# Kernel optimization log

Measured on AMD Instinct MI355X. Metric: run time of the kernel, lower is better.

The kernel has to match this reference:

```python
import jax, jax.numpy as jnp
import numpy as np

N = 8192
IN_F = 512
OUT_F = 128
ALPHA = 0.2  # leaky relu negative slope
NEG_BIG = -1e10
RND_SCALE = 1e5


def setup_inputs() -> dict:
    key = jax.random.key(0)
    k1, k2, k3, k4, k5 = jax.random.split(key, 5)
    h = jax.random.normal(k1, (N, IN_F), dtype=jnp.float32)
    adj = jax.random.randint(k2, (N, N), 0, 2, dtype=jnp.int32)
    W = jax.random.normal(k3, (IN_F, OUT_F), dtype=jnp.float32) * 0.05
    a = jax.random.normal(k4, (2 * OUT_F, 1), dtype=jnp.float32) * 0.1
    # rnd in original is 1e5*(rand-0.5); same distribution here
    rnd = RND_SCALE * (jax.random.uniform(k5, (N, OUT_F), dtype=jnp.float32) - 0.5)
    return {"h": h, "adj": adj, "W": W, "a": a, "rnd": rnd}


def reference(h, adj, W, a, rnd):
    Wh = h @ W                              # [N, OUT_F]
    Wh1 = Wh @ a[:OUT_F, :]                 # [N, 1]
    Wh2 = Wh @ a[OUT_F:, :]                 # [N, 1]
    e = jax.nn.leaky_relu(Wh1 + Wh2.T, negative_slope=ALPHA)  # [N, N]
    attention = jnp.where(adj > 0, e, NEG_BIG)
    attention = jax.nn.softmax(attention, axis=1)
    h_prime = attention @ Wh                # [N, OUT_F]
    h_prime = (h_prime + rnd) / RND_SCALE
    return jax.nn.elu(h_prime)
```

## Files before the change

### kernel.cpp

```cpp
#include <hip/hip_runtime.h>

#define N 8192
#define IN_F 512
#define OUT_F 128
#define NW (N / 8)
#define SPLITK 8
#define KC 1024
#define LOG2E 1.4426950408889634f
#define LN2 0.6931471805599453f

typedef __attribute__((ext_vector_type(4))) float f32x4;
typedef __attribute__((ext_vector_type(8))) short bf16x8;
typedef __attribute__((ext_vector_type(8))) unsigned short u16x8;
typedef __attribute__((ext_vector_type(4))) int i32x4;

__device__ __forceinline__ short f2bf(float f) {
    union { float f; unsigned u; } c; c.f = f;
    unsigned r = c.u + 0x7FFFu + ((c.u >> 16) & 1u);
    return (short)(r >> 16);
}

__device__ __forceinline__ float exp2fast(float x) {
#if __has_builtin(__builtin_amdgcn_exp2f)
    return __builtin_amdgcn_exp2f(x);
#else
    return __expf(x * LN2);
#endif
}

__device__ __forceinline__ void load_lds16(const void* g, void* l) {
    __builtin_amdgcn_global_load_lds((const __attribute__((address_space(1))) unsigned*)g,
                                     (__attribute__((address_space(3))) unsigned*)l,
                                     16, 0, 0);
}

__global__ __launch_bounds__(256) void prep(const int* __restrict__ adj,
                                            unsigned char* __restrict__ maskR,
                                            const float* __restrict__ W,
                                            short* __restrict__ WT) {
    if (blockIdx.x >= 2048) {
        int idx = (blockIdx.x - 2048) * 256 + threadIdx.x;
        int n = idx & (OUT_F - 1);
        int k = idx >> 7;
        WT[(size_t)n * IN_F + k] = f2bf(W[idx]);
        return;
    }
    const int wave = threadIdx.x >> 6, lane = threadIdx.x & 63;
    const size_t m = (size_t)blockIdx.x * 4 + wave;
    const i32x4* ap = (const i32x4*)(adj + m * N);
    unsigned char* mp = maskR + m * NW;
#pragma unroll 4
    for (int it = 0; it < 16; it++) {
        int b4 = it * 128 + lane * 2;
        i32x4 a0 = __builtin_nontemporal_load(ap + b4);
        i32x4 a1 = __builtin_nontemporal_load(ap + b4 + 1);
        unsigned b = (unsigned)(a0.x > 0) | ((unsigned)(a0.y > 0) << 1) |
                     ((unsigned)(a0.z > 0) << 2) | ((unsigned)(a0.w > 0) << 3) |
                     ((unsigned)(a1.x > 0) << 4) | ((unsigned)(a1.y > 0) << 5) |
                     ((unsigned)(a1.z > 0) << 6) | ((unsigned)(a1.w > 0) << 7);
        mp[it * 64 + lane] = (unsigned char)b;
    }
}

__global__ __launch_bounds__(256) void gemm_hW(const float* __restrict__ h,
                                               const short* __restrict__ WT,
                                               const float* __restrict__ a,
                                               short* __restrict__ WhT,
                                               float* __restrict__ sOut,
                                               float* __restrict__ tOut) {
    const int tid = threadIdx.x;
    const int wave = tid >> 6, lane = tid & 63;
    const int row16 = lane & 15, kgrp = lane >> 4;
    const int m0 = blockIdx.x * 16;
    const int kbase = wave * 128;

    f32x4 acc[8] = {};
    const float4* hp = (const float4*)(h + (size_t)(m0 + row16) * IN_F + kbase);

#pragma unroll
    for (int kk = 0; kk < 128; kk += 32) {
        float4 u0 = hp[kk / 4 + kgrp * 2];
        float4 u1 = hp[kk / 4 + kgrp * 2 + 1];
        bf16x8 af;
        af[0] = f2bf(u0.x); af[1] = f2bf(u0.y); af[2] = f2bf(u0.z); af[3] = f2bf(u0.w);
        af[4] = f2bf(u1.x); af[5] = f2bf(u1.y); af[6] = f2bf(u1.z); af[7] = f2bf(u1.w);
#pragma unroll
        for (int nt = 0; nt < 8; nt++) {
            bf16x8 bf_ = *(const bf16x8*)(WT + (size_t)(nt * 16 + row16) * IN_F + kbase + kk + kgrp * 8);
            acc[nt] = __builtin_amdgcn_mfma_f32_16x16x32_bf16(af, bf_, acc[nt], 0, 0, 0);
        }
    }

    __shared__ float red[4][16][132];
#pragma unroll
    for (int nt = 0; nt < 8; nt++)
#pragma unroll
        for (int r = 0; r < 4; r++)
            red[wave][kgrp * 4 + r][nt * 16 + row16] = acc[nt][r];
    __syncthreads();

    const int row = tid >> 4, seg = tid & 15;
    float v[8];
#pragma unroll
    for (int e = 0; e < 8; e++) {
        int c = seg * 8 + e;
        v[e] = red[0][row][c] + red[1][row][c] + red[2][row][c] + red[3][row][c];
    }
    float sp = 0.f, tp = 0.f;
#pragma unroll
    for (int e = 0; e < 8; e++) {
        sp += v[e] * a[seg * 8 + e];
        tp += v[e] * a[OUT_F + seg * 8 + e];
    }
    sp += __shfl_xor(sp, 1); tp += __shfl_xor(tp, 1);
    sp += __shfl_xor(sp, 2); tp += __shfl_xor(tp, 2);
    sp += __shfl_xor(sp, 4); tp += __shfl_xor(tp, 4);
    sp += __shfl_xor(sp, 8); tp += __shfl_xor(tp, 8);
    if (seg == 0) {
        sOut[m0 + row] = sp * LOG2E;
        tOut[m0 + row] = tp * LOG2E;
    }
#pragma unroll
    for (int e = 0; e < 8; e++)
        WhT[(size_t)(seg * 8 + e) * N + m0 + row] = f2bf(v[e]);
}

__global__ __launch_bounds__(256, 4) void attn(const unsigned char* __restrict__ maskR,
                                               const short* __restrict__ WhT,
                                               const float* __restrict__ s,
                                               const float* __restrict__ t,
                                               unsigned short* __restrict__ num,
                                               float* __restrict__ lpart) {
    const int tid = threadIdx.x;
    const int wave = tid >> 6, lane = tid & 63;
    const int row16 = lane & 15, kgrp = lane >> 4;
    const int kb = blockIdx.x & 7;
    const int mb = blockIdx.x >> 3;
    const int m0 = mb * 64 + wave * 16;
    const int m  = m0 + row16;
    const int ks = kb * KC;

    __shared__ short Bs[2][2][128 * 32];
    __shared__ float tl[KC];

    for (int i = tid; i < KC; i += 256) tl[i] = t[ks + i];

    const float s_m = s[m];
    const int4* mp = (const int4*)(maskR + (size_t)m * NW + (ks >> 3));
    int4 mcur = mp[0], mnxt = mp[1];

    auto stageB = [&](int sup, int par) {
        const int k0 = ks + sup * 64;
#pragma unroll
        for (int d = 0; d < 2; d++)
#pragma unroll
            for (int q = 0; q < 2; q++) {
                int nrow = wave * 32 + q * 16 + (lane >> 2);
                const short* g = WhT + (size_t)nrow * N + k0 + d * 32 + (lane & 3) * 8;
                load_lds16(g, &Bs[par][d][(wave * 32 + q * 16) * 32]);
            }
    };

    f32x4 acc[8] = {};
    float lsum = 0.f;

    stageB(0, 0);
    __syncthreads();

    for (int sp2 = 0; sp2 < 8; sp2++) {
#pragma unroll
        for (int ss = 0; ss < 2; ss++) {
            const int sp = sp2 * 2 + ss;
            const int par = sp & 1;
            if (sp + 1 < 16) stageB(sp + 1, par ^ 1);
#pragma unroll
            for (int d = 0; d < 2; d++) {
                const int g = sp * 2 + d;
                const unsigned dw = (unsigned)((const int*)&mcur)[ss * 2 + d];
                const unsigned mbyte = (dw >> (kgrp * 8)) & 0xFFu;

                const float* tp = tl + g * 32 + kgrp * 8;
                float4 tA = *(const float4*)tp;
                float4 tB = *(const float4*)(tp + 4);
                float tv[8] = { tA.x, tA.y, tA.z, tA.w, tB.x, tB.y, tB.z, tB.w };

                bf16x8 bfr[8];
                const short* base = &Bs[par][d][0];
#pragma unroll
                for (int ni = 0; ni < 8; ni++)
                    bfr[ni] = *(const bf16x8*)(base + (ni * 16 + row16) * 32 + kgrp * 8);

                unsigned pu[8];
#pragma unroll
                for (int e = 0; e < 8; e++) {
                    float x = s_m + tv[e];
                    x = fmaxf(x, 0.2f * x);
                    float p = exp2fast(x);
                    unsigned u = __float_as_uint(p) & 0xFFFF0000u;
                    u = ((mbyte >> e) & 1u) ? u : 0u;
                    lsum += __uint_as_float(u);
                    pu[e] = u;
                }
                bf16x8 af;
                unsigned* au = (unsigned*)&af;
#pragma unroll
                for (int q = 0; q < 4; q++) au[q] = (pu[2 * q] >> 16) | pu[2 * q + 1];
#pragma unroll
                for (int ni = 0; ni < 8; ni++)
                    acc[ni] = __builtin_amdgcn_mfma_f32_16x16x32_bf16(af, bfr[ni], acc[ni], 0, 0, 0);
            }
            __syncthreads();
        }
        mcur = mnxt;
        if (sp2 + 2 < 8) mnxt = mp[sp2 + 2];
    }

    {
        float v = lsum;
        v += __shfl_xor(v, 16);
        v += __shfl_xor(v, 32);
        if (kgrp == 0) lpart[(size_t)kb * N + m] = v;
    }

    unsigned short* np_ = num + ((size_t)kb * N + m0) * OUT_F;
#pragma unroll
    for (int ni = 0; ni < 8; ni++) {
        int n = ni * 16 + row16;
#pragma unroll
        for (int r = 0; r < 4; r++)
            np_[(size_t)(kgrp * 4 + r) * OUT_F + n] = (unsigned short)f2bf(acc[ni][r]);
    }
}

__global__ __launch_bounds__(256) void finalize(const unsigned short* __restrict__ num,
                                                const float* __restrict__ lpart,
                                                const float* __restrict__ rnd,
                                                float* __restrict__ out) {
    int idx = blockIdx.x * 256 + threadIdx.x;
    int m = idx >> 4;
    int c = (idx & 15) * 8;
    size_t g = (size_t)m * OUT_F + c;

    float nm[8] = {};
#pragma unroll
    for (int bk = 0; bk < SPLITK; bk++) {
        u16x8 v = *(const u16x8*)(num + (size_t)bk * N * OUT_F + g);
#pragma unroll
        for (int e = 0; e < 8; e++) nm[e] += __uint_as_float((unsigned)v[e] << 16);
    }
    float l = 0.f;
#pragma unroll
    for (int bk = 0; bk < SPLITK; bk++) l += lpart[(size_t)bk * N + m];
    float inv = 1.f / fmaxf(l, 1e-30f);

    float4 r0 = *(const float4*)(rnd + g);
    float4 r1 = *(const float4*)(rnd + g + 4);
    float rv[8] = { r0.x, r0.y, r0.z, r0.w, r1.x, r1.y, r1.z, r1.w };
    float ov[8];
#pragma unroll
    for (int e = 0; e < 8; e++) {
        float x = (nm[e] * inv + rv[e]) * 1e-5f;
        ov[e] = x > 0.f ? x : __expf(x) - 1.f;
    }
    *(float4*)(out + g)     = make_float4(ov[0], ov[1], ov[2], ov[3]);
    *(float4*)(out + g + 4) = make_float4(ov[4], ov[5], ov[6], ov[7]);
}

extern "C" void kernel_launch(void* const* d_in, const int* in_sizes, int n_in,
                              void* d_out, int out_size, void* d_ws, size_t ws_size,
                              hipStream_t stream) {
    const float* h   = (const float*)d_in[0];
    const int*   adj = (const int*)d_in[1];
    const float* W   = (const float*)d_in[2];
    const float* a   = (const float*)d_in[3];
    const float* rnd = (const float*)d_in[4];
    float* out = (float*)d_out;

    char* w = (char*)d_ws;
    short* WT    = (short*)(w);
    short* WhT   = (short*)(w + 131072);
    float* sv    = (float*)(w + 2228224);
    float* tv    = (float*)(w + 2260992);
    float* lpart = (float*)(w + 2293760);
    unsigned char* maskR = (unsigned char*)(w + 2555904);
    unsigned short* num  = (unsigned short*)(w + 10944512);

    prep    <<<2304, 256, 0, stream>>>(adj, maskR, W, WT);
    gemm_hW <<<512, 256, 0, stream>>>(h, WT, a, WhT, sv, tv);
    attn    <<<1024, 256, 0, stream>>>(maskR, WhT, sv, tv, num, lpart);
    finalize<<<(N * OUT_F / 8) / 256, 256, 0, stream>>>(num, lpart, rnd, out);
}
```

Before: 410.0 us.

## Fuse adjacency mask reading into attention kernel, drop bitmask prep pass

Removes the separate pass that packs the int32 adjacency matrix into a bitmask and instead has the attention kernel read the raw adj values directly, prefetched one stage ahead with nontemporal loads. This cuts the extra write and read of the packed mask and one kernel's worth of work, so the 256 MB adjacency is streamed once. The catch is that the attention kernel now pulls 32x more mask bytes per element and carries more live registers for the prefetch buffers, which may hurt occupancy or stall the MFMA loop.

```diff
diff --git a/kernel.cpp b/kernel.cpp
--- a/kernel.cpp
+++ b/kernel.cpp
@@ -3,7 +3,6 @@
 #define N 8192
 #define IN_F 512
 #define OUT_F 128
-#define NW (N / 8)
 #define SPLITK 8
 #define KC 1024
 #define LOG2E 1.4426950408889634f
@@ -34,32 +33,12 @@
                                      16, 0, 0);
 }
 
-__global__ __launch_bounds__(256) void prep(const int* __restrict__ adj,
-                                            unsigned char* __restrict__ maskR,
-                                            const float* __restrict__ W,
+__global__ __launch_bounds__(256) void prep(const float* __restrict__ W,
                                             short* __restrict__ WT) {
-    if (blockIdx.x >= 2048) {
-        int idx = (blockIdx.x - 2048) * 256 + threadIdx.x;
-        int n = idx & (OUT_F - 1);
-        int k = idx >> 7;
-        WT[(size_t)n * IN_F + k] = f2bf(W[idx]);
-        return;
-    }
-    const int wave = threadIdx.x >> 6, lane = threadIdx.x & 63;
-    const size_t m = (size_t)blockIdx.x * 4 + wave;
-    const i32x4* ap = (const i32x4*)(adj + m * N);
-    unsigned char* mp = maskR + m * NW;
-#pragma unroll 4
-    for (int it = 0; it < 16; it++) {
-        int b4 = it * 128 + lane * 2;
-        i32x4 a0 = __builtin_nontemporal_load(ap + b4);
-        i32x4 a1 = __builtin_nontemporal_load(ap + b4 + 1);
-        unsigned b = (unsigned)(a0.x > 0) | ((unsigned)(a0.y > 0) << 1) |
-                     ((unsigned)(a0.z > 0) << 2) | ((unsigned)(a0.w > 0) << 3) |
-                     ((unsigned)(a1.x > 0) << 4) | ((unsigned)(a1.y > 0) << 5) |
-                     ((unsigned)(a1.z > 0) << 6) | ((unsigned)(a1.w > 0) << 7);
-        mp[it * 64 + lane] = (unsigned char)b;
-    }
+    int idx = blockIdx.x * 256 + threadIdx.x;
+    int n = idx & (OUT_F - 1);
+    int k = idx >> 7;
+    WT[(size_t)n * IN_F + k] = f2bf(W[idx]);
 }
 
 __global__ __launch_bounds__(256) void gemm_hW(const float* __restrict__ h,
@@ -125,7 +104,7 @@
         WhT[(size_t)(seg * 8 + e) * N + m0 + row] = f2bf(v[e]);
 }
 
-__global__ __launch_bounds__(256, 4) void attn(const unsigned char* __restrict__ maskR,
+__global__ __launch_bounds__(256, 4) void attn(const int* __restrict__ adj,
                                                const short* __restrict__ WhT,
                                                const float* __restrict__ s,
                                                const float* __restrict__ t,
@@ -143,11 +122,18 @@
     __shared__ short Bs[2][2][128 * 32];
     __shared__ float tl[KC];
 
+    const i32x4* ap = (const i32x4*)(adj + (size_t)m * N + ks);
+    const int abase = kgrp * 2;
+
+    i32x4 ab[2][4];
+#pragma unroll
+    for (int d = 0; d < 2; d++)
+#pragma unroll
+        for (int hh = 0; hh < 2; hh++)
+            ab[0][d * 2 + hh] = __builtin_nontemporal_load(ap + d * 8 + abase + hh);
+
     for (int i = tid; i < KC; i += 256) tl[i] = t[ks + i];
-
     const float s_m = s[m];
-    const int4* mp = (const int4*)(maskR + (size_t)m * NW + (ks >> 3));
-    int4 mcur = mp[0], mnxt = mp[1];
 
     auto stageB = [&](int sup, int par) {
         const int k0 = ks + sup * 64;
@@ -167,17 +153,25 @@
     stageB(0, 0);
     __syncthreads();
 
-    for (int sp2 = 0; sp2 < 8; sp2++) {
+    for (int spo = 0; spo < 8; spo++) {
 #pragma unroll
         for (int ss = 0; ss < 2; ss++) {
-            const int sp = sp2 * 2 + ss;
-            const int par = sp & 1;
-            if (sp + 1 < 16) stageB(sp + 1, par ^ 1);
+            const int sp = spo * 2 + ss;
+            const int par = ss;
+            if (sp + 1 < 16) {
+#pragma unroll
+                for (int d = 0; d < 2; d++)
+#pragma unroll
+                    for (int hh = 0; hh < 2; hh++)
+                        ab[ss ^ 1][d * 2 + hh] =
+                            __builtin_nontemporal_load(ap + (sp + 1) * 16 + d * 8 + abase + hh);
+                stageB(sp + 1, par ^ 1);
+            }
 #pragma unroll
             for (int d = 0; d < 2; d++) {
                 const int g = sp * 2 + d;
-                const unsigned dw = (unsigned)((const int*)&mcur)[ss * 2 + d];
-                const unsigned mbyte = (dw >> (kgrp * 8)) & 0xFFu;
+                const i32x4 a0 = ab[ss][d * 2 + 0];
+                const i32x4 a1 = ab[ss][d * 2 + 1];
 
                 const float* tp = tl + g * 32 + kgrp * 8;
                 float4 tA = *(const float4*)tp;
@@ -190,29 +184,31 @@
                 for (int ni = 0; ni < 8; ni++)
                     bfr[ni] = *(const bf16x8*)(base + (ni * 16 + row16) * 32 + kgrp * 8);
 
-                unsigned pu[8];
-#pragma unroll
-                for (int e = 0; e < 8; e++) {
-                    float x = s_m + tv[e];
-                    x = fmaxf(x, 0.2f * x);
-                    float p = exp2fast(x);
-                    unsigned u = __float_as_uint(p) & 0xFFFF0000u;
-                    u = ((mbyte >> e) & 1u) ? u : 0u;
-                    lsum += __uint_as_float(u);
-                    pu[e] = u;
-                }
                 bf16x8 af;
                 unsigned* au = (unsigned*)&af;
 #pragma unroll
-                for (int q = 0; q < 4; q++) au[q] = (pu[2 * q] >> 16) | pu[2 * q + 1];
+                for (int q = 0; q < 4; q++) {
+                    const int e0 = 2 * q, e1 = 2 * q + 1;
+                    float x0 = s_m + tv[e0];
+                    float x1 = s_m + tv[e1];
+                    x0 = fmaxf(x0, 0.2f * x0);
+                    x1 = fmaxf(x1, 0.2f * x1);
+                    unsigned u0 = __float_as_uint(exp2fast(x0)) & 0xFFFF0000u;
+                    unsigned u1 = __float_as_uint(exp2fast(x1)) & 0xFFFF0000u;
+                    const int av0 = (e0 < 4) ? a0[e0] : a1[e0 - 4];
+                    const int av1 = (e1 < 4) ? a0[e1] : a1[e1 - 4];
+                    u0 = av0 > 0 ? u0 : 0u;
+                    u1 = av1 > 0 ? u1 : 0u;
+                    lsum += __uint_as_float(u0);
+                    lsum += __uint_as_float(u1);
+                    au[q] = (u0 >> 16) | u1;
+                }
 #pragma unroll
                 for (int ni = 0; ni < 8; ni++)
                     acc[ni] = __builtin_amdgcn_mfma_f32_16x16x32_bf16(af, bfr[ni], acc[ni], 0, 0, 0);
             }
             __syncthreads();
         }
-        mcur = mnxt;
-        if (sp2 + 2 < 8) mnxt = mp[sp2 + 2];
     }
 
     {
@@ -282,11 +278,10 @@
     float* sv    = (float*)(w + 2228224);
     float* tv    = (float*)(w + 2260992);
     float* lpart = (float*)(w + 2293760);
-    unsigned char* maskR = (unsigned char*)(w + 2555904);
-    unsigned short* num  = (unsigned short*)(w + 10944512);
-
-    prep    <<<2304, 256, 0, stream>>>(adj, maskR, W, WT);
+    unsigned short* num  = (unsigned short*)(w + 2555904);
+
+    prep    <<<256, 256, 0, stream>>>(W, WT);
     gemm_hW <<<512, 256, 0, stream>>>(h, WT, a, WhT, sv, tv);
-    attn    <<<1024, 256, 0, stream>>>(maskR, WhT, sv, tv, num, lpart);
-    finalize<<<(N * OUT_F / 8) / 256, 256, 0, stream>>>(num, lpart, rnd, out);
-}
+    attn    <<<1024, 256, 0, stream>>>(adj, WhT, sv, tv, num, lpart);
+    finalize<<<512, 256, 0, stream>>>(num, lpart, rnd, out);
+}
```

Measured after the change: 423.5 us. +3.3%, slower.

## Pre-pack Wh into MFMA fragment layout and fuse mask build with h@W GEMM

Applied to the files above, without the earlier changes.

The h@W GEMM now writes Wh in a packed layout that matches the attention kernel's MFMA B-fragment order. The attention kernel can then stage each tile with contiguous global-to-LDS copies and read B fragments with a linear lane*8 stride instead of strided row loads. The adjacency-to-bitmask conversion moves out of prep into the same launch as the GEMM, so the bandwidth-heavy mask pass runs alongside the GEMM. prep now only transposes W. The cost is scattered 2-byte stores when writing the packed buffer.

```diff
diff --git a/kernel.cpp b/kernel.cpp
--- a/kernel.cpp
+++ b/kernel.cpp
@@ -3,9 +3,9 @@
 #define N 8192
 #define IN_F 512
 #define OUT_F 128
-#define NW (N / 8)
 #define SPLITK 8
 #define KC 1024
+#define NW (N / 8)
 #define LOG2E 1.4426950408889634f
 #define LN2 0.6931471805599453f
 
@@ -34,40 +34,40 @@
                                      16, 0, 0);
 }
 
-__global__ __launch_bounds__(256) void prep(const int* __restrict__ adj,
-                                            unsigned char* __restrict__ maskR,
-                                            const float* __restrict__ W,
+__global__ __launch_bounds__(256) void prep(const float* __restrict__ W,
                                             short* __restrict__ WT) {
-    if (blockIdx.x >= 2048) {
-        int idx = (blockIdx.x - 2048) * 256 + threadIdx.x;
-        int n = idx & (OUT_F - 1);
-        int k = idx >> 7;
-        WT[(size_t)n * IN_F + k] = f2bf(W[idx]);
+    int idx = blockIdx.x * 256 + threadIdx.x;
+    int n = idx & (OUT_F - 1);
+    int k = idx >> 7;
+    WT[(size_t)n * IN_F + k] = f2bf(W[idx]);
+}
+
+__global__ __launch_bounds__(256) void gmask(const float* __restrict__ h,
+                                             const short* __restrict__ WT,
+                                             const float* __restrict__ a,
+                                             const int* __restrict__ adj,
+                                             short* __restrict__ Bpack,
+                                             float* __restrict__ sOut,
+                                             float* __restrict__ tOut,
+                                             unsigned char* __restrict__ maskR) {
+    if (blockIdx.x >= 512) {
+        const int wave = threadIdx.x >> 6, lane = threadIdx.x & 63;
+        const size_t m = (size_t)(blockIdx.x - 512) * 4 + wave;
+        const i32x4* ap = (const i32x4*)(adj + m * N);
+        unsigned char* mp = maskR + m * NW;
+#pragma unroll 4
+        for (int it = 0; it < 16; it++) {
+            int b4 = it * 128 + lane * 2;
+            i32x4 a0 = __builtin_nontemporal_load(ap + b4);
+            i32x4 a1 = __builtin_nontemporal_load(ap + b4 + 1);
+            unsigned b = (unsigned)(a0.x > 0) | ((unsigned)(a0.y > 0) << 1) |
+                         ((unsigned)(a0.z > 0) << 2) | ((unsigned)(a0.w > 0) << 3) |
+                         ((unsigned)(a1.x > 0) << 4) | ((unsigned)(a1.y > 0) << 5) |
+                         ((unsigned)(a1.z > 0) << 6) | ((unsigned)(a1.w > 0) << 7);
+            mp[it * 64 + lane] = (unsigned char)b;
+        }
         return;
     }
-    const int wave = threadIdx.x >> 6, lane = threadIdx.x & 63;
-    const size_t m = (size_t)blockIdx.x * 4 + wave;
-    const i32x4* ap = (const i32x4*)(adj + m * N);
-    unsigned char* mp = maskR + m * NW;
-#pragma unroll 4
-    for (int it = 0; it < 16; it++) {
-        int b4 = it * 128 + lane * 2;
-        i32x4 a0 = __builtin_nontemporal_load(ap + b4);
-        i32x4 a1 = __builtin_nontemporal_load(ap + b4 + 1);
-        unsigned b = (unsigned)(a0.x > 0) | ((unsigned)(a0.y > 0) << 1) |
-                     ((unsigned)(a0.z > 0) << 2) | ((unsigned)(a0.w > 0) << 3) |
-                     ((unsigned)(a1.x > 0) << 4) | ((unsigned)(a1.y > 0) << 5) |
-                     ((unsigned)(a1.z > 0) << 6) | ((unsigned)(a1.w > 0) << 7);
-        mp[it * 64 + lane] = (unsigned char)b;
-    }
-}
-
-__global__ __launch_bounds__(256) void gemm_hW(const float* __restrict__ h,
-                                               const short* __restrict__ WT,
-                                               const float* __restrict__ a,
-                                               short* __restrict__ WhT,
-                                               float* __restrict__ sOut,
-                                               float* __restrict__ tOut) {
     const int tid = threadIdx.x;
     const int wave = tid >> 6, lane = tid & 63;
     const int row16 = lane & 15, kgrp = lane >> 4;
@@ -120,13 +120,21 @@
         sOut[m0 + row] = sp * LOG2E;
         tOut[m0 + row] = tp * LOG2E;
     }
-#pragma unroll
-    for (int e = 0; e < 8; e++)
-        WhT[(size_t)(seg * 8 + e) * N + m0 + row] = f2bf(v[e]);
+
+    {
+        const int k = m0 + row;
+        const int G = k >> 5;
+        const int ksub = (k >> 3) & 3;
+        const int elem = k & 7;
+        short* bp = Bpack + ((size_t)(G * 8 + (seg >> 1)) * 64 + ksub * 16 + (seg & 1) * 8) * 8 + elem;
+#pragma unroll
+        for (int e = 0; e < 8; e++)
+            bp[e * 8] = f2bf(v[e]);
+    }
 }
 
 __global__ __launch_bounds__(256, 4) void attn(const unsigned char* __restrict__ maskR,
-                                               const short* __restrict__ WhT,
+                                               const short* __restrict__ Bpack,
                                                const float* __restrict__ s,
                                                const float* __restrict__ t,
                                                unsigned short* __restrict__ num,
@@ -140,7 +148,7 @@
     const int m  = m0 + row16;
     const int ks = kb * KC;
 
-    __shared__ short Bs[2][2][128 * 32];
+    __shared__ __align__(16) short Bs[2][8192];
     __shared__ float tl[KC];
 
     for (int i = tid; i < KC; i += 256) tl[i] = t[ks + i];
@@ -150,15 +158,11 @@
     int4 mcur = mp[0], mnxt = mp[1];
 
     auto stageB = [&](int sup, int par) {
-        const int k0 = ks + sup * 64;
-#pragma unroll
-        for (int d = 0; d < 2; d++)
-#pragma unroll
-            for (int q = 0; q < 2; q++) {
-                int nrow = wave * 32 + q * 16 + (lane >> 2);
-                const short* g = WhT + (size_t)nrow * N + k0 + d * 32 + (lane & 3) * 8;
-                load_lds16(g, &Bs[par][d][(wave * 32 + q * 16) * 32]);
-            }
+        const short* src = Bpack + (size_t)(kb * 32 + sup * 2) * 4096;
+#pragma unroll
+        for (int it = 0; it < 4; it++)
+            load_lds16(src + it * 2048 + wave * 512 + lane * 8,
+                       &Bs[par][it * 2048 + wave * 512]);
     };
 
     f32x4 acc[8] = {};
@@ -171,7 +175,7 @@
 #pragma unroll
         for (int ss = 0; ss < 2; ss++) {
             const int sp = sp2 * 2 + ss;
-            const int par = sp & 1;
+            const int par = ss;
             if (sp + 1 < 16) stageB(sp + 1, par ^ 1);
 #pragma unroll
             for (int d = 0; d < 2; d++) {
@@ -185,10 +189,9 @@
                 float tv[8] = { tA.x, tA.y, tA.z, tA.w, tB.x, tB.y, tB.z, tB.w };
 
                 bf16x8 bfr[8];
-                const short* base = &Bs[par][d][0];
 #pragma unroll
                 for (int ni = 0; ni < 8; ni++)
-                    bfr[ni] = *(const bf16x8*)(base + (ni * 16 + row16) * 32 + kgrp * 8);
+                    bfr[ni] = *(const bf16x8*)(&Bs[par][d * 4096 + ni * 512 + lane * 8]);
 
                 unsigned pu[8];
 #pragma unroll
@@ -278,15 +281,15 @@
 
     char* w = (char*)d_ws;
     short* WT    = (short*)(w);
-    short* WhT   = (short*)(w + 131072);
+    short* Bpack = (short*)(w + 131072);
     float* sv    = (float*)(w + 2228224);
     float* tv    = (float*)(w + 2260992);
     float* lpart = (float*)(w + 2293760);
-    unsigned char* maskR = (unsigned char*)(w + 2555904);
-    unsigned short* num  = (unsigned short*)(w + 10944512);
-
-    prep    <<<2304, 256, 0, stream>>>(adj, maskR, W, WT);
-    gemm_hW <<<512, 256, 0, stream>>>(h, WT, a, WhT, sv, tv);
-    attn    <<<1024, 256, 0, stream>>>(maskR, WhT, sv, tv, num, lpart);
-    finalize<<<(N * OUT_F / 8) / 256, 256, 0, stream>>>(num, lpart, rnd, out);
-}
+    unsigned short* num  = (unsigned short*)(w + 2555904);
+    unsigned char* maskR = (unsigned char*)(w + 19333120);
+
+    prep    <<<256, 256, 0, stream>>>(W, WT);
+    gmask   <<<2560, 256, 0, stream>>>(h, WT, a, adj, Bpack, sv, tv, maskR);
+    attn    <<<1024, 256, 0, stream>>>(maskR, Bpack, sv, tv, num, lpart);
+    finalize<<<512, 256, 0, stream>>>(num, lpart, rnd, out);
+}
```

After: 408.8 us (median of 2 runs). Within noise of the previous version (-0.3%).
